# Optimization experiments

Measured on AMD Instinct MI355X. Metric: run time of the kernel, lower is better.

Reference implementation:

```python
import jax, jax.numpy as jnp
from jax import lax
import numpy as np

B = 4096        # num_batch
NVAR = 120      # 3 * num_legs(4) * horizon(10)
NC = 2 * NVAR   # num_constraints = 240
HID = 1024      # GRU hidden size
RIN = 3 * (NC + NVAR)  # GRU input dim = 1080
MAXITER = 8
RHO = 1.0
REG = 1e-4


def setup_inputs() -> dict:
    key = jax.random.key(0)
    ks = jax.random.split(key, 10)
    # SPD quadratic cost H, linear cost g, inequality constraints C x <= c
    M = jax.random.normal(ks[0], (NVAR, NVAR), jnp.float32)
    H = M @ M.T / NVAR + jnp.eye(NVAR, dtype=jnp.float32)
    g = jax.random.normal(ks[1], (NVAR,), jnp.float32)
    C = 0.1 * jax.random.normal(ks[2], (NC, NVAR), jnp.float32)
    c = jax.random.uniform(ks[3], (NC,), jnp.float32, 0.1, 1.0)
    lamda_init = jax.random.normal(ks[4], (B, NVAR), jnp.float32)
    s_init = jax.random.uniform(ks[5], (B, NC), jnp.float32)
    h_0 = jnp.zeros((B, HID), jnp.float32)
    # GRU cell (torch GRUCell layout: [3*HID, in]) + output head to NC+NVAR
    sc_i = 1.0 / np.sqrt(RIN)
    sc_h = 1.0 / np.sqrt(HID)
    W_ih = sc_i * jax.random.normal(ks[6], (3 * HID, RIN), jnp.float32)
    b_ih = jnp.zeros((3 * HID,), jnp.float32)
    W_hh = sc_h * jax.random.normal(ks[7], (3 * HID, HID), jnp.float32)
    b_hh = jnp.zeros((3 * HID,), jnp.float32)
    W_out = sc_h * jax.random.normal(ks[8], (NC + NVAR, HID), jnp.float32)
    b_out = jnp.zeros((NC + NVAR,), jnp.float32)
    return dict(lamda_init=lamda_init, s_init=s_init, h_0=h_0, H=H, g=g, C=C, c=c,
                W_ih=W_ih, b_ih=b_ih, W_hh=W_hh, b_hh=b_hh, W_out=W_out, b_out=b_out)


def _gru_cell(x, h, W_ih, b_ih, W_hh, b_hh):
    gi = x @ W_ih.T + b_ih
    gh = h @ W_hh.T + b_hh
    i_r, i_z, i_n = jnp.split(gi, 3, axis=1)
    h_r, h_z, h_n = jnp.split(gh, 3, axis=1)
    r = jax.nn.sigmoid(i_r + h_r)
    z = jax.nn.sigmoid(i_z + h_z)
    n = jnp.tanh(i_n + r * h_n)
    return (1.0 - z) * n + z * h


def reference(lamda_init, s_init, h_0, H, g, C, c, W_ih, b_ih, W_hh, b_hh, W_out, b_out):
    I = jnp.eye(NVAR, dtype=H.dtype)
    # ---- init solve (compute_projection_gru preamble) ----
    Q_inv0 = jnp.linalg.pinv(H + REG * I)
    lincost0 = -0.0 * lamda_init + g                 # [B, NVAR]
    xi0 = (-lincost0) @ Q_inv0.T                     # sol = (Qinv @ rhs.T).T
    s0 = jnp.maximum(0.0, -(xi0 @ C.T) + c)
    s0 = 0.0 * s_init + s0                           # s_init = 0*nn + 1*s_
    lam0 = lamda_init
    # ---- constant per-iteration projection matrix (same every iter) ----
    Q_inv = jnp.linalg.pinv(H + RHO * (C.T @ C) + REG * I)

    def step(carry, _):
        s, lam, h = carry
        # compute_feasible_control
        b_aug = c - s                                # [B, NC]
        lincost = -lam + g - RHO * (b_aug @ C)       # [B, NVAR]
        xi = (-lincost) @ Q_inv.T                    # [B, NVAR]
        Axi = xi @ C.T                               # [B, NC]
        s_new = jnp.maximum(0.0, -Axi + c)
        res_vec = Axi - c + s_new
        res_norm = jnp.linalg.norm(res_vec, axis=1)
        lam_new = lam - RHO * (res_vec @ C)
        qp_cost = 0.5 * (xi @ H @ xi.T) + xi @ g     # [B, B] (faithful to source)
        qp_norm = jnp.linalg.norm(qp_cost, axis=1)
        # GRU refinement
        r = jnp.concatenate([s, lam, s_new, lam_new, s_new - s, lam_new - lam], axis=1)
        h_new = _gru_cell(r, h, W_ih, b_ih, W_hh, b_hh)
        out = h_new @ W_out.T + b_out                # [B, NC+NVAR]
        s_fin = jnp.maximum(0.0, s_new + out[:, :NC])
        lam_fin = lam_new + out[:, NC:NC + NVAR]
        fixed = jnp.linalg.norm(lam - lam_fin, axis=1) + jnp.linalg.norm(s - s_fin, axis=1)
        return (s_fin, lam_fin, h_new), (xi, res_norm, fixed, qp_norm)

    (_, _, _), (xis, primal, fixed, qpres) = lax.scan(step, (s0, lam0, h_0), None, length=MAXITER)
    return xis[-1], primal, fixed, qpres
```

## Files before the change

kernel.cpp:

```cpp
#include <hip/hip_runtime.h>
#include <hip/hip_bf16.h>
#include <math.h>

#define NB    4096
#define NV    120
#define NCN   240
#define HIDD  1024
#define RINN  1080
#define NOUTD 360
#define NOUTP 384
#define NITER 8
#define REGEPS 1e-4f
#define NPART 128

#define KCAT 4224
#define HOFF 2176
#define KWC  2112
#define KWO  1024
#define NSTEP_R 34
#define NSTEPS  66

typedef unsigned short u16;
typedef __attribute__((ext_vector_type(8))) short short8v;
typedef __attribute__((ext_vector_type(4))) float f32x4;

__device__ inline u16 f2b(float x) {
    __hip_bfloat16 h = __float2bfloat16(x);
    return __builtin_bit_cast(u16, h);
}
__device__ inline float b2f(u16 u) {
    __hip_bfloat16 h = __builtin_bit_cast(__hip_bfloat16, u);
    return __bfloat162float(h);
}

__device__ inline void gl16(const void* g, void* l) {
    __builtin_amdgcn_global_load_lds(
        (__attribute__((address_space(1))) void*)(void*)g,
        (__attribute__((address_space(3))) void*)l, 16, 0, 0);
}

__global__ void k_buildA(const float* __restrict__ H, const float* __restrict__ C,
                         float* __restrict__ A, float* __restrict__ A0) {
    int i = blockIdx.x;
    int which = blockIdx.y;
    for (int j = threadIdx.x; j < NV; j += blockDim.x) {
        float v = H[i*NV + j] + (i == j ? REGEPS : 0.f);
        if (which == 0) {
            float acc = 0.f;
            for (int k = 0; k < NCN; ++k) acc += C[k*NV + i] * C[k*NV + j];
            A[i*NV + j] = v + acc;
        } else {
            A0[i*NV + j] = v;
        }
    }
}

__device__ inline void inv4x4(const float* m, float* inv) {
    float s0 = m[0]*m[5] - m[1]*m[4];
    float s1 = m[0]*m[6] - m[2]*m[4];
    float s2 = m[0]*m[7] - m[3]*m[4];
    float s3 = m[1]*m[6] - m[2]*m[5];
    float s4 = m[1]*m[7] - m[3]*m[5];
    float s5 = m[2]*m[7] - m[3]*m[6];
    float c5 = m[10]*m[15] - m[11]*m[14];
    float c4 = m[9]*m[15] - m[11]*m[13];
    float c3 = m[9]*m[14] - m[10]*m[13];
    float c2 = m[8]*m[15] - m[11]*m[12];
    float c1 = m[8]*m[14] - m[10]*m[12];
    float c0 = m[8]*m[13] - m[9]*m[12];
    float det = s0*c5 - s1*c4 + s2*c3 + s3*c2 - s4*c1 + s5*c0;
    float id = 1.0f / det;
    inv[0]  = ( m[5]*c5 - m[6]*c4 + m[7]*c3) * id;
    inv[1]  = (-m[1]*c5 + m[2]*c4 - m[3]*c3) * id;
    inv[2]  = ( m[13]*s5 - m[14]*s4 + m[15]*s3) * id;
    inv[3]  = (-m[9]*s5 + m[10]*s4 - m[11]*s3) * id;
    inv[4]  = (-m[4]*c5 + m[6]*c2 - m[7]*c1) * id;
    inv[5]  = ( m[0]*c5 - m[2]*c2 + m[3]*c1) * id;
    inv[6]  = (-m[12]*s5 + m[14]*s2 - m[15]*s1) * id;
    inv[7]  = ( m[8]*s5 - m[10]*s2 + m[11]*s1) * id;
    inv[8]  = ( m[4]*c4 - m[5]*c2 + m[7]*c0) * id;
    inv[9]  = (-m[0]*c4 + m[1]*c2 - m[3]*c0) * id;
    inv[10] = ( m[12]*s4 - m[13]*s2 + m[15]*s0) * id;
    inv[11] = (-m[8]*s4 + m[9]*s2 - m[11]*s0) * id;
    inv[12] = (-m[4]*c3 + m[5]*c1 - m[6]*c0) * id;
    inv[13] = ( m[0]*c3 - m[1]*c1 + m[2]*c0) * id;
    inv[14] = (-m[12]*s3 + m[13]*s1 - m[14]*s0) * id;
    inv[15] = ( m[8]*s3 - m[9]*s1 + m[10]*s0) * id;
}

__global__ __launch_bounds__(1024) void k_invert(const float* __restrict__ Ain,
                                                 const float* __restrict__ A0in,
                                                 float* __restrict__ Qi,
                                                 float* __restrict__ Qi0) {
    __shared__ float M[NV][132];
    __shared__ float Rl[4][132];
    __shared__ float Bl[16];
    const float* src = (blockIdx.x == 0) ? Ain : A0in;
    float* dst = (blockIdx.x == 0) ? Qi : Qi0;
    const int t = threadIdx.x;
    for (int idx = t; idx < NV*132; idx += 1024) {
        int i = idx / 132, j = idx - i*132;
        M[i][j] = (j < NV) ? src[i*NV + j] : 0.f;
    }
    __syncthreads();
    const int ty = t >> 5;
    const int g4 = (t & 31) * 4;
    for (int kk = 0; kk < NV; kk += 4) {
        if (ty == 0) {
            float a[16], b[16];
            #pragma unroll
            for (int p = 0; p < 4; ++p) {
                float4 v = *(const float4*)&M[kk + p][kk];
                a[p*4+0] = v.x; a[p*4+1] = v.y; a[p*4+2] = v.z; a[p*4+3] = v.w;
            }
            inv4x4(a, b);
            float4 m0v = *(const float4*)&M[kk+0][g4];
            float4 m1v = *(const float4*)&M[kk+1][g4];
            float4 m2v = *(const float4*)&M[kk+2][g4];
            float4 m3v = *(const float4*)&M[kk+3][g4];
            #pragma unroll
            for (int p = 0; p < 4; ++p) {
                float4 r;
                r.x = b[p*4+0]*m0v.x + b[p*4+1]*m1v.x + b[p*4+2]*m2v.x + b[p*4+3]*m3v.x;
                r.y = b[p*4+0]*m0v.y + b[p*4+1]*m1v.y + b[p*4+2]*m2v.y + b[p*4+3]*m3v.y;
                r.z = b[p*4+0]*m0v.z + b[p*4+1]*m1v.z + b[p*4+2]*m2v.z + b[p*4+3]*m3v.z;
                r.w = b[p*4+0]*m0v.w + b[p*4+1]*m1v.w + b[p*4+2]*m2v.w + b[p*4+3]*m3v.w;
                *(float4*)&Rl[p][g4] = r;
            }
            if (t < 16) Bl[t] = b[t];
        }
        float4 F[4];
        #pragma unroll
        for (int q = 0; q < 4; ++q) {
            int i = ty + 32*q;
            F[q] = (i < NV) ? *(const float4*)&M[i][kk] : float4{0.f,0.f,0.f,0.f};
        }
        __syncthreads();
        #pragma unroll
        for (int q = 0; q < 4; ++q) {
            int i = ty + 32*q;
            if (i < NV) {
                int dp = i - kk;
                bool ispiv = (dp >= 0) && (dp < 4);
                float4 v;
                if (g4 == kk) {
                    if (ispiv) {
                        v = *(const float4*)&Bl[dp*4];
                    } else {
                        v.x = -(F[q].x*Bl[0] + F[q].y*Bl[4] + F[q].z*Bl[8]  + F[q].w*Bl[12]);
                        v.y = -(F[q].x*Bl[1] + F[q].y*Bl[5] + F[q].z*Bl[9]  + F[q].w*Bl[13]);
                        v.z = -(F[q].x*Bl[2] + F[q].y*Bl[6] + F[q].z*Bl[10] + F[q].w*Bl[14]);
                        v.w = -(F[q].x*Bl[3] + F[q].y*Bl[7] + F[q].z*Bl[11] + F[q].w*Bl[15]);
                    }
                } else if (ispiv) {
                    v = *(const float4*)&Rl[dp][g4];
                } else {
                    float4 r0 = *(const float4*)&Rl[0][g4];
                    float4 r1 = *(const float4*)&Rl[1][g4];
                    float4 r2 = *(const float4*)&Rl[2][g4];
                    float4 r3 = *(const float4*)&Rl[3][g4];
                    v = *(const float4*)&M[i][g4];
                    v.x -= F[q].x*r0.x + F[q].y*r1.x + F[q].z*r2.x + F[q].w*r3.x;
                    v.y -= F[q].x*r0.y + F[q].y*r1.y + F[q].z*r2.y + F[q].w*r3.y;
                    v.z -= F[q].x*r0.z + F[q].y*r1.z + F[q].z*r2.z + F[q].w*r3.z;
                    v.w -= F[q].x*r0.w + F[q].y*r1.w + F[q].z*r2.w + F[q].w*r3.w;
                }
                *(float4*)&M[i][g4] = v;
            }
        }
        __syncthreads();
    }
    for (int idx = t; idx < NV*NV; idx += 1024) {
        int i = idx / NV, j = idx - i*NV;
        dst[idx] = M[i][j];
    }
}

__global__ void k_s0(const float* __restrict__ Qi0, const float* __restrict__ g,
                     const float* __restrict__ C, const float* __restrict__ c,
                     float* __restrict__ s0v) {
    __shared__ float xi0[NV];
    int t = threadIdx.x;
    if (t < NV) {
        float a = 0.f;
        for (int j = 0; j < NV; ++j) a += Qi0[t*NV + j] * g[j];
        xi0[t] = -a;
    }
    __syncthreads();
    if (t < NCN) {
        float a = 0.f;
        for (int j = 0; j < NV; ++j) a += C[t*NV + j] * xi0[j];
        s0v[t] = fmaxf(0.f, c[t] - a);
    }
}

__global__ void k_init(const float* __restrict__ s0v, const float* __restrict__ lam0,
                       float* __restrict__ s, float* __restrict__ lam) {
    int b0 = blockIdx.x * 8;
    int t = threadIdx.x;
    for (int idx = t; idx < 8*NCN; idx += 256) {
        int m = idx / NCN, k = idx % NCN;
        s[(size_t)(b0 + m)*NCN + k] = s0v[k];
    }
    for (int idx = t; idx < 8*NV; idx += 256) lam[(size_t)b0*NV + idx] = lam0[(size_t)b0*NV + idx];
}

__global__ void k_packH(const float* __restrict__ h0, u16* __restrict__ act) {
    int n = blockIdx.x;
    size_t base = (size_t)n * KCAT + HOFF;
    for (int k = threadIdx.x; k < HIDD; k += 256) {
        float x = h0[(size_t)n * HIDD + k];
        u16 hi = f2b(x);
        act[base + k] = hi;
        act[base + HIDD + k] = f2b(x - b2f(hi));
    }
}

__global__ void k_packWcat(const float* __restrict__ Wih, const float* __restrict__ Whh,
                           u16* __restrict__ Wc) {
    int n = blockIdx.x;
    size_t base = (size_t)n * KWC;
    for (int k = threadIdx.x; k < 1088; k += 256)
        Wc[base + k] = f2b(k < RINN ? Wih[(size_t)n * RINN + k] : 0.f);
    for (int k = threadIdx.x; k < HIDD; k += 256)
        Wc[base + 1088 + k] = f2b(Whh[(size_t)n * HIDD + k]);
}

__global__ void k_packWo(const float* __restrict__ src, u16* __restrict__ dst) {
    int n = blockIdx.x;
    size_t row = (size_t)n * KWO;
    for (int k = threadIdx.x; k < KWO; k += 256)
        dst[row + k] = f2b(n < NOUTD ? src[(size_t)n * HIDD + k] : 0.f);
}

__device__ inline void write2(u16* __restrict__ act, size_t base, int pos, float x) {
    u16 hi = f2b(x);
    u16 lo = f2b(x - b2f(hi));
    act[base + pos] = hi;
    act[base + 1088 + pos] = lo;
}

__global__ __launch_bounds__(512) void k_xiproj(
        const float* __restrict__ s, const float* __restrict__ lam,
        const float* __restrict__ C, const float* __restrict__ c,
        const float* __restrict__ g, const float* __restrict__ Qi,
        const float* __restrict__ H,
        float* __restrict__ xi, float* __restrict__ Y, float* __restrict__ wv,
        float* __restrict__ snew, float* __restrict__ lamn,
        u16* __restrict__ act, float* __restrict__ primal) {
    __shared__ float bd[16][NCN];
    __shared__ float ul[16][NV];
    __shared__ float xl[16][NV];
    __shared__ float resl[16][NCN];
    int b0 = blockIdx.x * 16;
    int t = threadIdx.x;
    for (int idx = t; idx < 16*NCN; idx += 512) {
        int m = idx / NCN, k = idx % NCN;
        bd[m][k] = c[k] - s[(size_t)(b0 + m)*NCN + k];
    }
    __syncthreads();
    for (int idx = t; idx < 16*NV; idx += 512) {
        int m = idx / NV, j = idx % NV;
        float a = lam[(size_t)(b0 + m)*NV + j] - g[j];
        for (int k = 0; k < NCN; ++k) a += bd[m][k] * C[k*NV + j];
        ul[m][j] = a;
    }
    __syncthreads();
    for (int idx = t; idx < 16*NV; idx += 512) {
        int m = idx / NV, i = idx % NV;
        float a = 0.f;
        for (int j = 0; j < NV; ++j) a += Qi[j*NV + i] * ul[m][j];
        xl[m][i] = a;
        xi[(size_t)(b0 + m)*NV + i] = a;
    }
    __syncthreads();
    for (int idx = t; idx < 16*NV; idx += 512) {
        int m = idx / NV, i = idx % NV;
        float a = 0.f;
        for (int j = 0; j < NV; ++j) a += xl[m][j] * H[j*NV + i];
        Y[(size_t)(b0 + m)*NV + i] = a;
    }
    if (t < 16) {
        float a = 0.f;
        for (int j = 0; j < NV; ++j) a += xl[t][j] * g[j];
        wv[b0 + t] = a;
    }
    for (int idx = t; idx < 16*NCN; idx += 512) {
        int m = idx / NCN, k = idx % NCN;
        float a = 0.f;
        for (int j = 0; j < NV; ++j) a += C[k*NV + j] * xl[m][j];
        float sn = fmaxf(0.f, c[k] - a);
        float rv = a - c[k] + sn;
        resl[m][k] = rv;
        int b = b0 + m;
        snew[(size_t)b*NCN + k] = sn;
        float so = s[(size_t)b*NCN + k];
        size_t base = (size_t)b * KCAT;
        write2(act, base, k, so);
        write2(act, base, 360 + k, sn);
        write2(act, base, 720 + k, sn - so);
    }
    __syncthreads();
    if (t < 16) {
        float a = 0.f;
        for (int k = 0; k < NCN; ++k) a += resl[t][k] * resl[t][k];
        primal[b0 + t] = sqrtf(a);
    }
    for (int idx = t; idx < 16*NV; idx += 512) {
        int m = idx / NV, i = idx % NV;
        float a = 0.f;
        for (int k = 0; k < NCN; ++k) a += resl[m][k] * C[k*NV + i];
        int b = b0 + m;
        float lo = lam[(size_t)b*NV + i];
        float ln = lo - a;
        lamn[(size_t)b*NV + i] = ln;
        size_t base = (size_t)b * KCAT;
        write2(act, base, 240 + i, lo);
        write2(act, base, 600 + i, ln);
        write2(act, base, 960 + i, ln - lo);
    }
    for (int idx = t; idx < 16*8; idx += 512) {
        int m = idx >> 3, k = 1080 + (idx & 7);
        size_t base = (size_t)(b0 + m) * KCAT;
        act[base + k] = 0;
        act[base + 1088 + k] = 0;
    }
}

__global__ __launch_bounds__(256) void k_qp_part(const float* __restrict__ xi, const float* __restrict__ wv,
                         double* __restrict__ Gp, double* __restrict__ vp, double* __restrict__ Sp) {
    __shared__ float xl[32][NV];
    __shared__ float wl[32];
    int p = blockIdx.x;
    int b0 = p * 32;
    int t = threadIdx.x;
    for (int idx = t; idx < 32*NV; idx += 256) xl[idx/NV][idx%NV] = xi[(size_t)b0*NV + idx];
    if (t < 32) wl[t] = wv[b0 + t];
    __syncthreads();
    for (int idx = t; idx < NV*NV; idx += 256) {
        int i = idx / NV, j = idx % NV;
        double a = 0.0;
        for (int m = 0; m < 32; ++m) a += (double)xl[m][i] * (double)xl[m][j];
        Gp[(size_t)p*NV*NV + idx] = a;
    }
    if (t < NV) {
        double a = 0.0;
        for (int m = 0; m < 32; ++m) a += (double)wl[m] * (double)xl[m][t];
        vp[(size_t)p*NV + t] = a;
    }
    if (t == 0) {
        double a = 0.0;
        for (int m = 0; m < 32; ++m) a += (double)wl[m] * (double)wl[m];
        Sp[p] = a;
    }
}

__global__ void k_qp_red(const double* __restrict__ Gp, const double* __restrict__ vp,
                         const double* __restrict__ Sp,
                         double* __restrict__ G, double* __restrict__ v, double* __restrict__ S) {
    int idx = blockIdx.x * 256 + threadIdx.x;
    if (idx < NV*NV) {
        double a = 0.0;
        for (int p = 0; p < NPART; ++p) a += Gp[(size_t)p*NV*NV + idx];
        G[idx] = a;
    }
    if (idx < NV) {
        double a = 0.0;
        for (int p = 0; p < NPART; ++p) a += vp[(size_t)p*NV + idx];
        v[idx] = a;
    }
    if (idx == 0) {
        double a = 0.0;
        for (int p = 0; p < NPART; ++p) a += Sp[p];
        S[0] = a;
    }
}

__global__ __launch_bounds__(256) void k_qp_norm(const float* __restrict__ Y, const double* __restrict__ G,
                         const double* __restrict__ v, const double* __restrict__ S,
                         float* __restrict__ qp) {
    __shared__ float Yl[16][NV];
    __shared__ double tl[16][NV];
    int b0 = blockIdx.x * 16;
    int t = threadIdx.x;
    for (int idx = t; idx < 16*NV; idx += 256) Yl[idx/NV][idx%NV] = Y[(size_t)b0*NV + idx];
    __syncthreads();
    for (int idx = t; idx < 16*NV; idx += 256) {
        int m = idx / NV, i = idx % NV;
        double a = 0.0;
        for (int j = 0; j < NV; ++j) a += G[j*NV + i] * (double)Yl[m][j];
        tl[m][i] = a;
    }
    __syncthreads();
    if (t < 16) {
        double a = 0.0, bv = 0.0;
        for (int i = 0; i < NV; ++i) { a += (double)Yl[t][i] * tl[t][i]; bv += (double)Yl[t][i] * v[i]; }
        double q = 0.25 * a + bv + S[0];
        qp[b0 + t] = (float)sqrt(q > 0.0 ? q : 0.0);
    }
}

#define GRUF_STEP(NSLOT, BUFI) do {                                              \
    char* Ah_ = lds + (BUFI) * 40960;                                            \
    char* Al_ = Ah_ + 8192;                                                      \
    char* Bb_ = Ah_ + 16384;                                                     \
    const int srow = lane & 15;                                                  \
    const int ksl = lane >> 4;                                                   \
    short8v ah[4], al[4];                                                        \
    _Pragma("unroll")                                                            \
    for (int fm = 0; fm < 4; ++fm) {                                             \
        int rr = wm * 64 + fm * 16 + srow;                                       \
        int off = rr * 64 + ((ksl ^ ((rr >> 1) & 3)) << 4);                      \
        ah[fm] = *(const short8v*)(Ah_ + off);                                   \
        al[fm] = *(const short8v*)(Al_ + off);                                   \
    }                                                                            \
    _Pragma("unroll")                                                            \
    for (int fn = 0; fn < 2; ++fn) {                                             \
        int rb = wn * 32 + fn * 16 + srow;                                       \
        int boff = rb * 64 + ((ksl ^ ((rb >> 1) & 3)) << 4);                     \
        short8v bfr = *(const short8v*)(Bb_ + boff);                             \
        short8v bfz = *(const short8v*)(Bb_ + 8192 + boff);                      \
        short8v bfn = *(const short8v*)(Bb_ + 16384 + boff);                     \
        _Pragma("unroll")                                                        \
        for (int fm = 0; fm < 4; ++fm) {                                         \
            acc[0][fn][fm] = __builtin_amdgcn_mfma_f32_16x16x32_bf16(ah[fm], bfr, acc[0][fn][fm], 0, 0, 0); \
            acc[0][fn][fm] = __builtin_amdgcn_mfma_f32_16x16x32_bf16(al[fm], bfr, acc[0][fn][fm], 0, 0, 0); \
            acc[1][fn][fm] = __builtin_amdgcn_mfma_f32_16x16x32_bf16(ah[fm], bfz, acc[1][fn][fm], 0, 0, 0); \
            acc[1][fn][fm] = __builtin_amdgcn_mfma_f32_16x16x32_bf16(al[fm], bfz, acc[1][fn][fm], 0, 0, 0); \
            acc[NSLOT][fn][fm] = __builtin_amdgcn_mfma_f32_16x16x32_bf16(ah[fm], bfn, acc[NSLOT][fn][fm], 0, 0, 0); \
            acc[NSLOT][fn][fm] = __builtin_amdgcn_mfma_f32_16x16x32_bf16(al[fm], bfn, acc[NSLOT][fn][fm], 0, 0, 0); \
        }                                                                        \
    }                                                                            \
} while (0)

#define GRUF_SYNC5 do {                                                          \
    asm volatile("s_waitcnt vmcnt(5)" ::: "memory");                             \
    __builtin_amdgcn_s_barrier();                                                \
    __builtin_amdgcn_sched_barrier(0);                                           \
} while (0)
#define GRUF_SYNC0 do {                                                          \
    asm volatile("s_waitcnt vmcnt(0)" ::: "memory");                             \
    __builtin_amdgcn_s_barrier();                                                \
    __builtin_amdgcn_sched_barrier(0);                                           \
} while (0)

__global__ __launch_bounds__(512, 2) void k_gruf(
        const u16* __restrict__ act,
        const u16* __restrict__ Wc,
        const float* __restrict__ bih, const float* __restrict__ bhh,
        u16* __restrict__ actn) {
    __shared__ char lds[122880];
    const int t = threadIdx.x;
    const int lane = t & 63;
    const int wid = t >> 6;
    const int wm = wid >> 2;
    const int wn = wid & 3;
    const int bid = blockIdx.x;
    const int xcd = bid & 7;
    const int slot = bid >> 3;
    const int m0 = (xcd * 4 + (slot & 3)) * 128;
    const int n0 = (slot >> 2) * 128;

    f32x4 acc[4][2][4];
    #pragma unroll
    for (int i = 0; i < 4; ++i)
        #pragma unroll
        for (int j = 0; j < 2; ++j)
            #pragma unroll
            for (int k = 0; k < 4; ++k) {
                f32x4 z = {0.f, 0.f, 0.f, 0.f};
                acc[i][j][k] = z;
            }

    auto stage = [&](int step) {
        char* Ah_ = lds + (step % 3) * 40960;
        char* Al_ = Ah_ + 8192;
        char* Bb_ = Ah_ + 16384;
        const int hiOff = (step < NSTEP_R) ? step * 32 : step * 32 + 1088;
        const int loOff = hiOff + ((step < NSTEP_R) ? 1088 : 1024);
        const int wOff = step * 32;
        {
            int s = (wid << 6) + lane;
            int rr = s >> 2;
            int kq = ((lane & 3) ^ ((rr >> 1) & 3)) << 3;
            gl16(act + (size_t)(m0 + rr) * KCAT + hiOff + kq, Ah_ + wid * 1024);
            gl16(act + (size_t)(m0 + rr) * KCAT + loOff + kq, Al_ + wid * 1024);
        }
        #pragma unroll
        for (int q = 0; q < 3; ++q) {
            int cb = q * 8 + wid;
            int s2 = (cb << 6) + lane;
            int rbg = s2 >> 2;
            int kq = ((lane & 3) ^ ((rbg >> 1) & 3)) << 3;
            gl16(Wc + (size_t)((rbg >> 7) * 1024 + n0 + (rbg & 127)) * KWC + wOff + kq,
                 Bb_ + cb * 1024);
        }
    };

    stage(0);
    stage(1);
    GRUF_SYNC5;
    for (int step = 0; step < NSTEP_R; ++step) {
        stage(step + 2);
        GRUF_STEP(2, step % 3);
        GRUF_SYNC5;
    }
    for (int step = NSTEP_R; step < NSTEPS; ++step) {
        if (step + 2 < NSTEPS) {
            stage(step + 2);
            GRUF_STEP(3, step % 3);
            GRUF_SYNC5;
        } else {
            GRUF_STEP(3, step % 3);
            GRUF_SYNC0;
        }
    }

    #pragma unroll
    for (int fn = 0; fn < 2; ++fn) {
        const int jj = n0 + wn * 32 + fn * 16 + (lane & 15);
        const float bir = bih[jj],        bhr = bhh[jj];
        const float biz = bih[1024 + jj], bhz = bhh[1024 + jj];
        const float bin = bih[2048 + jj], bhn = bhh[2048 + jj];
        #pragma unroll
        for (int fm = 0; fm < 4; ++fm) {
            #pragma unroll
            for (int rg = 0; rg < 4; ++rg) {
                int m = m0 + wm * 64 + fm * 16 + (lane >> 4) * 4 + rg;
                float rz = acc[0][fn][fm][rg];
                float zz = acc[1][fn][fm][rg];
                float inn = acc[2][fn][fm][rg];
                float hnn = acc[3][fn][fm][rg];
                float rgate = 1.f / (1.f + expf(-(rz + bir + bhr)));
                float zgate = 1.f / (1.f + expf(-(zz + biz + bhz)));
                float ngate = tanhf(inn + bin + rgate * (hnn + bhn));
                size_t base = (size_t)m * KCAT + HOFF;
                float hv = b2f(act[base + jj]) + b2f(act[base + HIDD + jj]);
                float hnew = (1.f - zgate) * ngate + zgate * hv;
                u16 nh = f2b(hnew);
                actn[base + jj] = nh;
                actn[base + HIDD + jj] = f2b(hnew - b2f(nh));
            }
        }
    }
}

__global__ __launch_bounds__(512, 2) void k_outp(
        const u16* __restrict__ act, const u16* __restrict__ Wo,
        const float* __restrict__ bo, float* __restrict__ outb) {
    __shared__ char lds[49152];
    const int t = threadIdx.x;
    const int lane = t & 63;
    const int wid = t >> 6;
    const int wm = wid >> 2;
    const int wn = wid & 3;
    const int m0 = blockIdx.x * 128;
    const int n0 = blockIdx.y * 128;
    f32x4 acc[2][4];
    #pragma unroll
    for (int i = 0; i < 2; ++i)
        #pragma unroll
        for (int j = 0; j < 4; ++j) {
            f32x4 z = {0.f, 0.f, 0.f, 0.f};
            acc[i][j] = z;
        }

    auto stage = [&](int step, int buf) {
        char* Ah_ = lds + buf * 24576;
        char* Al_ = Ah_ + 8192;
        char* Bb_ = Ah_ + 16384;
        const int hiOff = HOFF + step * 32;
        const int loOff = HOFF + HIDD + step * 32;
        int s = (wid << 6) + lane;
        int rr = s >> 2;
        int kq = ((lane & 3) ^ ((rr >> 1) & 3)) << 3;
        gl16(act + (size_t)(m0 + rr) * KCAT + hiOff + kq, Ah_ + wid * 1024);
        gl16(act + (size_t)(m0 + rr) * KCAT + loOff + kq, Al_ + wid * 1024);
        gl16(Wo + (size_t)(n0 + rr) * KWO + step * 32 + kq, Bb_ + wid * 1024);
    };

    stage(0, 0);
    __syncthreads();
    int cur = 0;
    for (int step = 0; step < 32; ++step) {
        if (step + 1 < 32) stage(step + 1, cur ^ 1);
        {
            char* Ah_ = lds + cur * 24576;
            char* Al_ = Ah_ + 8192;
            char* Bb_ = Ah_ + 16384;
            const int srow = lane & 15;
            const int ksl = lane >> 4;
            short8v ah[4], al[4];
            #pragma unroll
            for (int fm = 0; fm < 4; ++fm) {
                int rr = wm * 64 + fm * 16 + srow;
                int off = rr * 64 + ((ksl ^ ((rr >> 1) & 3)) << 4);
                ah[fm] = *(const short8v*)(Ah_ + off);
                al[fm] = *(const short8v*)(Al_ + off);
            }
            #pragma unroll
            for (int fn = 0; fn < 2; ++fn) {
                int rb = wn * 32 + fn * 16 + srow;
                int boff = rb * 64 + ((ksl ^ ((rb >> 1) & 3)) << 4);
                short8v bf = *(const short8v*)(Bb_ + boff);
                #pragma unroll
                for (int fm = 0; fm < 4; ++fm) {
                    acc[fn][fm] = __builtin_amdgcn_mfma_f32_16x16x32_bf16(ah[fm], bf, acc[fn][fm], 0, 0, 0);
                    acc[fn][fm] = __builtin_amdgcn_mfma_f32_16x16x32_bf16(al[fm], bf, acc[fn][fm], 0, 0, 0);
                }
            }
        }
        __syncthreads();
        cur ^= 1;
    }
    #pragma unroll
    for (int fn = 0; fn < 2; ++fn) {
        int n = n0 + wn * 32 + fn * 16 + (lane & 15);
        if (n < NOUTD) {
            float bb = bo[n];
            #pragma unroll
            for (int fm = 0; fm < 4; ++fm) {
                #pragma unroll
                for (int rg = 0; rg < 4; ++rg) {
                    int m = m0 + wm * 64 + fm * 16 + (lane >> 4) * 4 + rg;
                    outb[(size_t)m * NOUTP + n] = acc[fn][fm][rg] + bb;
                }
            }
        }
    }
}

__global__ __launch_bounds__(256) void k_fin(const float* __restrict__ snew, const float* __restrict__ lamn,
                     const float* __restrict__ outb,
                     float* __restrict__ s, float* __restrict__ lam,
                     float* __restrict__ fx) {
    __shared__ float redS[16][17];
    __shared__ float redL[16][17];
    int b0 = blockIdx.x * 16;
    int tm = threadIdx.x / 16;
    int tk = threadIdx.x % 16;
    int b = b0 + tm;
    float ds2 = 0.f, dl2 = 0.f;
    for (int k = tk; k < NCN; k += 16) {
        float o = outb[(size_t)b*NOUTP + k];
        float sf = fmaxf(0.f, snew[(size_t)b*NCN + k] + o);
        float so = s[(size_t)b*NCN + k];
        s[(size_t)b*NCN + k] = sf;
        float d = so - sf;
        ds2 += d * d;
    }
    for (int i = tk; i < NV; i += 16) {
        float o = outb[(size_t)b*NOUTP + NCN + i];
        float lf = lamn[(size_t)b*NV + i] + o;
        float lo = lam[(size_t)b*NV + i];
        lam[(size_t)b*NV + i] = lf;
        float d = lo - lf;
        dl2 += d * d;
    }
    redS[tm][tk] = ds2;
    redL[tm][tk] = dl2;
    __syncthreads();
    if (tk == 0) {
        float a = 0.f, l = 0.f;
        for (int q = 0; q < 16; ++q) { a += redS[tm][q]; l += redL[tm][q]; }
        fx[b] = sqrtf(l) + sqrtf(a);
    }
}

extern "C" void kernel_launch(void* const* d_in, const int* in_sizes, int n_in,
                              void* d_out, int out_size, void* d_ws, size_t ws_size,
                              hipStream_t stream) {
    const float* lamda_init = (const float*)d_in[0];
    const float* h0    = (const float*)d_in[2];
    const float* H     = (const float*)d_in[3];
    const float* g     = (const float*)d_in[4];
    const float* C     = (const float*)d_in[5];
    const float* c     = (const float*)d_in[6];
    const float* W_ih  = (const float*)d_in[7];
    const float* b_ih  = (const float*)d_in[8];
    const float* W_hh  = (const float*)d_in[9];
    const float* b_hh  = (const float*)d_in[10];
    const float* W_out = (const float*)d_in[11];
    const float* b_out = (const float*)d_in[12];

    float* out    = (float*)d_out;
    float* xi_out = out;
    float* primal = out + (size_t)NB*NV;
    float* fixedo = primal + (size_t)NITER*NB;
    float* qpres  = fixedo + (size_t)NITER*NB;

    char* wp = (char*)d_ws;
    auto alloc = [&](size_t bytes) {
        void* p = (void*)wp;
        wp += (bytes + 255) & ~(size_t)255;
        return p;
    };
    float* Amat  = (float*)alloc(NV*NV*4);
    float* A0m   = (float*)alloc(NV*NV*4);
    float* Qinv  = (float*)alloc(NV*NV*4);
    float* Qinv0 = (float*)alloc(NV*NV*4);
    float* s0v   = (float*)alloc(NCN*4);
    float* sbuf  = (float*)alloc((size_t)NB*NCN*4);
    float* snew  = (float*)alloc((size_t)NB*NCN*4);
    float* lam   = (float*)alloc((size_t)NB*NV*4);
    float* lamn  = (float*)alloc((size_t)NB*NV*4);
    float* xib   = (float*)alloc((size_t)NB*NV*4);
    float* Yb    = (float*)alloc((size_t)NB*NV*4);
    float* wb    = (float*)alloc(NB*4);
    float* outb  = (float*)alloc((size_t)NB*NOUTP*4);
    u16* actA    = (u16*)alloc((size_t)NB*KCAT*2);
    u16* actB    = (u16*)alloc((size_t)NB*KCAT*2);
    u16* Wcat    = (u16*)alloc((size_t)3072*KWC*2);
    u16* Wopk    = (u16*)alloc((size_t)NOUTP*KWO*2);
    double* Gpart = (double*)alloc((size_t)NPART*NV*NV*8);
    double* vpart = (double*)alloc((size_t)NPART*NV*8);
    double* Spart = (double*)alloc(NPART*8);
    double* Gfin  = (double*)alloc(NV*NV*8);
    double* vfin  = (double*)alloc(NV*8);
    double* Sfin  = (double*)alloc(8);

    k_buildA<<<dim3(NV, 2), dim3(128), 0, stream>>>(H, C, Amat, A0m);
    k_invert<<<dim3(2), dim3(1024), 0, stream>>>(Amat, A0m, Qinv, Qinv0);
    k_s0<<<dim3(1), dim3(256), 0, stream>>>(Qinv0, g, C, c, s0v);
    k_init<<<dim3(NB/8), dim3(256), 0, stream>>>(s0v, lamda_init, sbuf, lam);
    k_packWcat<<<dim3(3072), dim3(256), 0, stream>>>(W_ih, W_hh, Wcat);
    k_packWo<<<dim3(NOUTP), dim3(256), 0, stream>>>(W_out, Wopk);
    k_packH<<<dim3(NB), dim3(256), 0, stream>>>(h0, actA);

    u16* hc = actA;
    u16* hn2 = actB;
    for (int it = 0; it < NITER; ++it) {
        k_xiproj<<<dim3(NB/16), dim3(512), 0, stream>>>(sbuf, lam, C, c, g, Qinv, H,
                                                        xib, Yb, wb, snew, lamn, hc,
                                                        primal + (size_t)it*NB);
        k_qp_part<<<dim3(NPART), dim3(256), 0, stream>>>(xib, wb, Gpart, vpart, Spart);
        k_qp_red<<<dim3((NV*NV + 255)/256), dim3(256), 0, stream>>>(Gpart, vpart, Spart, Gfin, vfin, Sfin);
        k_qp_norm<<<dim3(NB/16), dim3(256), 0, stream>>>(Yb, Gfin, vfin, Sfin, qpres + (size_t)it*NB);
        k_gruf<<<dim3(256), dim3(512), 0, stream>>>(hc, Wcat, b_ih, b_hh, hn2);
        k_outp<<<dim3(NB/128, 3), dim3(512), 0, stream>>>(hn2, Wopk, b_out, outb);
        k_fin<<<dim3(NB/16), dim3(256), 0, stream>>>(snew, lamn, outb, sbuf, lam, fixedo + (size_t)it*NB);
        u16* tmp = hc; hc = hn2; hn2 = tmp;
    }
    hipMemcpyAsync(xi_out, xib, (size_t)NB*NV*sizeof(float), hipMemcpyDeviceToDevice, stream);
}
```

Before: 2.586 ms.

## Double GRU kernel block to 1024 threads with warp-specialized loading and setprio

The fused GRU GEMM kernel now launches 16 waves per block instead of 8. Each wave computes a 32x32 sub-tile, halving per-wave accumulators and A-fragment loads. Loading is split by wave: waves 0-7 fetch weight tiles and waves 8-15 fetch activation hi/lo tiles, with per-group vmcnt waits. MFMA sections are wrapped in s_setprio to favour math issue. This trades more waves for latency hiding against fewer blocks per CU and more barrier participants.

```diff
diff --git a/kernel.cpp b/kernel.cpp
--- a/kernel.cpp
+++ b/kernel.cpp
@@ -406,14 +406,15 @@
     char* Bb_ = Ah_ + 16384;                                                     \
     const int srow = lane & 15;                                                  \
     const int ksl = lane >> 4;                                                   \
-    short8v ah[4], al[4];                                                        \
+    short8v ah[2], al[2];                                                        \
     _Pragma("unroll")                                                            \
-    for (int fm = 0; fm < 4; ++fm) {                                             \
-        int rr = wm * 64 + fm * 16 + srow;                                       \
+    for (int fm = 0; fm < 2; ++fm) {                                             \
+        int rr = wm * 32 + fm * 16 + srow;                                       \
         int off = rr * 64 + ((ksl ^ ((rr >> 1) & 3)) << 4);                      \
         ah[fm] = *(const short8v*)(Ah_ + off);                                   \
         al[fm] = *(const short8v*)(Al_ + off);                                   \
     }                                                                            \
+    __builtin_amdgcn_s_setprio(1);                                               \
     _Pragma("unroll")                                                            \
     for (int fn = 0; fn < 2; ++fn) {                                             \
         int rb = wn * 32 + fn * 16 + srow;                                       \
@@ -422,7 +423,7 @@
         short8v bfz = *(const short8v*)(Bb_ + 8192 + boff);                      \
         short8v bfn = *(const short8v*)(Bb_ + 16384 + boff);                     \
         _Pragma("unroll")                                                        \
-        for (int fm = 0; fm < 4; ++fm) {                                         \
+        for (int fm = 0; fm < 2; ++fm) {                                         \
             acc[0][fn][fm] = __builtin_amdgcn_mfma_f32_16x16x32_bf16(ah[fm], bfr, acc[0][fn][fm], 0, 0, 0); \
             acc[0][fn][fm] = __builtin_amdgcn_mfma_f32_16x16x32_bf16(al[fm], bfr, acc[0][fn][fm], 0, 0, 0); \
             acc[1][fn][fm] = __builtin_amdgcn_mfma_f32_16x16x32_bf16(ah[fm], bfz, acc[1][fn][fm], 0, 0, 0); \
@@ -431,10 +432,12 @@
             acc[NSLOT][fn][fm] = __builtin_amdgcn_mfma_f32_16x16x32_bf16(al[fm], bfn, acc[NSLOT][fn][fm], 0, 0, 0); \
         }                                                                        \
     }                                                                            \
+    __builtin_amdgcn_s_setprio(0);                                               \
 } while (0)
 
-#define GRUF_SYNC5 do {                                                          \
-    asm volatile("s_waitcnt vmcnt(5)" ::: "memory");                             \
+#define GRUF_SYNCN do {                                                          \
+    if (wid < 8) { asm volatile("s_waitcnt vmcnt(3)" ::: "memory"); }            \
+    else         { asm volatile("s_waitcnt vmcnt(2)" ::: "memory"); }            \
     __builtin_amdgcn_s_barrier();                                                \
     __builtin_amdgcn_sched_barrier(0);                                           \
 } while (0)
@@ -444,7 +447,7 @@
     __builtin_amdgcn_sched_barrier(0);                                           \
 } while (0)
 
-__global__ __launch_bounds__(512, 2) void k_gruf(
+__global__ __launch_bounds__(1024) void k_gruf(
         const u16* __restrict__ act,
         const u16* __restrict__ Wc,
         const float* __restrict__ bih, const float* __restrict__ bhh,
@@ -461,13 +464,13 @@
     const int m0 = (xcd * 4 + (slot & 3)) * 128;
     const int n0 = (slot >> 2) * 128;
 
-    f32x4 acc[4][2][4];
+    f32x4 acc[4][2][2];
     #pragma unroll
     for (int i = 0; i < 4; ++i)
         #pragma unroll
         for (int j = 0; j < 2; ++j)
             #pragma unroll
-            for (int k = 0; k < 4; ++k) {
+            for (int k = 0; k < 2; ++k) {
                 f32x4 z = {0.f, 0.f, 0.f, 0.f};
                 acc[i][j][k] = z;
             }
@@ -479,37 +482,37 @@
         const int hiOff = (step < NSTEP_R) ? step * 32 : step * 32 + 1088;
         const int loOff = hiOff + ((step < NSTEP_R) ? 1088 : 1024);
         const int wOff = step * 32;
-        {
-            int s = (wid << 6) + lane;
-            int rr = s >> 2;
+        if (wid >= 8) {
+            int q = wid - 8;
+            int rr = q * 16 + (lane >> 2);
             int kq = ((lane & 3) ^ ((rr >> 1) & 3)) << 3;
-            gl16(act + (size_t)(m0 + rr) * KCAT + hiOff + kq, Ah_ + wid * 1024);
-            gl16(act + (size_t)(m0 + rr) * KCAT + loOff + kq, Al_ + wid * 1024);
-        }
-        #pragma unroll
-        for (int q = 0; q < 3; ++q) {
-            int cb = q * 8 + wid;
-            int s2 = (cb << 6) + lane;
-            int rbg = s2 >> 2;
-            int kq = ((lane & 3) ^ ((rbg >> 1) & 3)) << 3;
-            gl16(Wc + (size_t)((rbg >> 7) * 1024 + n0 + (rbg & 127)) * KWC + wOff + kq,
-                 Bb_ + cb * 1024);
+            gl16(act + (size_t)(m0 + rr) * KCAT + hiOff + kq, Ah_ + q * 1024);
+            gl16(act + (size_t)(m0 + rr) * KCAT + loOff + kq, Al_ + q * 1024);
+        } else {
+            #pragma unroll
+            for (int j = 0; j < 3; ++j) {
+                int cb = wid * 3 + j;
+                int rbg = cb * 16 + (lane >> 2);
+                int kq = ((lane & 3) ^ ((rbg >> 1) & 3)) << 3;
+                gl16(Wc + (size_t)((rbg >> 7) * 1024 + n0 + (rbg & 127)) * KWC + wOff + kq,
+                     Bb_ + cb * 1024);
+            }
         }
     };
 
     stage(0);
     stage(1);
-    GRUF_SYNC5;
+    GRUF_SYNCN;
     for (int step = 0; step < NSTEP_R; ++step) {
         stage(step + 2);
         GRUF_STEP(2, step % 3);
-        GRUF_SYNC5;
+        GRUF_SYNCN;
     }
     for (int step = NSTEP_R; step < NSTEPS; ++step) {
         if (step + 2 < NSTEPS) {
             stage(step + 2);
             GRUF_STEP(3, step % 3);
-            GRUF_SYNC5;
+            GRUF_SYNCN;
         } else {
             GRUF_STEP(3, step % 3);
             GRUF_SYNC0;
@@ -523,10 +526,10 @@
         const float biz = bih[1024 + jj], bhz = bhh[1024 + jj];
         const float bin = bih[2048 + jj], bhn = bhh[2048 + jj];
         #pragma unroll
-        for (int fm = 0; fm < 4; ++fm) {
+        for (int fm = 0; fm < 2; ++fm) {
             #pragma unroll
             for (int rg = 0; rg < 4; ++rg) {
-                int m = m0 + wm * 64 + fm * 16 + (lane >> 4) * 4 + rg;
+                int m = m0 + wm * 32 + fm * 16 + (lane >> 4) * 4 + rg;
                 float rz = acc[0][fn][fm][rg];
                 float zz = acc[1][fn][fm][rg];
                 float inn = acc[2][fn][fm][rg];
@@ -736,7 +739,7 @@
         k_qp_part<<<dim3(NPART), dim3(256), 0, stream>>>(xib, wb, Gpart, vpart, Spart);
         k_qp_red<<<dim3((NV*NV + 255)/256), dim3(256), 0, stream>>>(Gpart, vpart, Spart, Gfin, vfin, Sfin);
         k_qp_norm<<<dim3(NB/16), dim3(256), 0, stream>>>(Yb, Gfin, vfin, Sfin, qpres + (size_t)it*NB);
-        k_gruf<<<dim3(256), dim3(512), 0, stream>>>(hc, Wcat, b_ih, b_hh, hn2);
+        k_gruf<<<dim3(256), dim3(1024), 0, stream>>>(hc, Wcat, b_ih, b_hh, hn2);
         k_outp<<<dim3(NB/128, 3), dim3(512), 0, stream>>>(hn2, Wopk, b_out, outb);
         k_fin<<<dim3(NB/16), dim3(256), 0, stream>>>(snew, lamn, outb, sbuf, lam, fixedo + (size_t)it*NB);
         u16* tmp = hc; hc = hn2; hn2 = tmp;
```

New measurement: 2.687 ms. 3.9% more time.
